# Optimization experiments

Hardware: AMD Instinct MI355X
Metric: run time of the kernel (lower is better)

Reference implementation:

```python
import jax, jax.numpy as jnp
import numpy as np

Cl, Nl, Cv, Nv, M = 32, 128, 8, 64, 500000


def _sample1d(line, g):
    # line: [C, N]; g in [-1,1]; align_corners=True, zeros padding
    C, N = line.shape
    ix = (g + 1.0) * 0.5 * (N - 1)
    i0 = jnp.floor(ix)
    w = ix - i0
    i0 = i0.astype(jnp.int32)
    def gth(i, wt):
        valid = (i >= 0) & (i < N)
        return line[:, jnp.clip(i, 0, N - 1)] * (wt * valid)
    return (gth(i0, 1.0 - w) + gth(i0 + 1, w)).T  # [M, C]


def _sample2d(plane, gx, gy):
    # plane: [C, H, W]; grid x -> W axis, y -> H axis (torch grid_sample convention)
    C, H, W = plane.shape
    ix = (gx + 1.0) * 0.5 * (W - 1)
    iy = (gy + 1.0) * 0.5 * (H - 1)
    x0 = jnp.floor(ix); y0 = jnp.floor(iy)
    wx = ix - x0; wy = iy - y0
    x0 = x0.astype(jnp.int32); y0 = y0.astype(jnp.int32)
    flat = plane.reshape(C, -1)
    def gth(xi, yi, wt):
        valid = (xi >= 0) & (xi < W) & (yi >= 0) & (yi < H)
        idx = jnp.clip(yi, 0, H - 1) * W + jnp.clip(xi, 0, W - 1)
        return flat[:, idx] * (wt * valid)
    out = (gth(x0, y0, (1 - wx) * (1 - wy)) + gth(x0 + 1, y0, wx * (1 - wy))
           + gth(x0, y0 + 1, (1 - wx) * wy) + gth(x0 + 1, y0 + 1, wx * wy))
    return out.T  # [M, C]


def _sample3d(vol, gx, gy, gz):
    # vol: [C, D, H, W]; grid (x,y,z) -> (W,H,D) axes
    C, D, H, W = vol.shape
    ix = (gx + 1.0) * 0.5 * (W - 1)
    iy = (gy + 1.0) * 0.5 * (H - 1)
    iz = (gz + 1.0) * 0.5 * (D - 1)
    x0 = jnp.floor(ix); y0 = jnp.floor(iy); z0 = jnp.floor(iz)
    wx = ix - x0; wy = iy - y0; wz = iz - z0
    x0 = x0.astype(jnp.int32); y0 = y0.astype(jnp.int32); z0 = z0.astype(jnp.int32)
    flat = vol.reshape(C, -1)
    out = 0.0
    for dz in (0, 1):
        for dy in (0, 1):
            for dx in (0, 1):
                xi, yi, zi = x0 + dx, y0 + dy, z0 + dz
                wt = ((wx if dx else 1 - wx) * (wy if dy else 1 - wy) * (wz if dz else 1 - wz))
                valid = (xi >= 0) & (xi < W) & (yi >= 0) & (yi < H) & (zi >= 0) & (zi < D)
                idx = (jnp.clip(zi, 0, D - 1) * H + jnp.clip(yi, 0, H - 1)) * W + jnp.clip(xi, 0, W - 1)
                out = out + flat[:, idx] * (wt * valid)
    return out.T  # [M, C]


def setup_inputs() -> dict:
    key = jax.random.key(0)
    ks = jax.random.split(key, 16)
    rng, shift = 0.4, 0.1
    coordinates = jax.random.uniform(ks[0], (1, M, 3), minval=-1.0, maxval=1.0)
    line_x = jax.random.uniform(ks[1], (Cl, Nl)) * rng + shift
    line_y = jax.random.uniform(ks[2], (Cl, Nl)) * rng + shift
    line_z = jax.random.uniform(ks[3], (Cl, Nl)) * rng + shift
    plane_xy = jax.random.normal(ks[4], (Cl, Nl, Nl)) * rng + shift
    plane_yz = jax.random.normal(ks[5], (Cl, Nl, Nl)) * rng + shift
    plane_xz = jax.random.normal(ks[6], (Cl, Nl, Nl)) * rng + shift
    volume = jax.random.normal(ks[7], (Cv, Nv, Nv, Nv)) * rng + shift
    def lin(k, fi, fo):
        k1, k2 = jax.random.split(k)
        lim = 1.0 / np.sqrt(fi)
        return (jax.random.uniform(k1, (fi, fo), minval=-lim, maxval=lim),
                jax.random.uniform(k2, (fo,), minval=-lim, maxval=lim))
    Wx, bx = lin(ks[8], Cl, Cl)
    Wy, by = lin(ks[9], Cl, Cl)
    Wz, bz = lin(ks[10], Cl, Cl)
    W1, b1 = lin(ks[11], Cl + Cv, 128)
    W2, b2 = lin(ks[12], 128, 1)
    return dict(coordinates=coordinates, line_x=line_x, line_y=line_y, line_z=line_z,
                plane_xy=plane_xy, plane_yz=plane_yz, plane_xz=plane_xz, volume=volume,
                Wx=Wx, bx=bx, Wy=Wy, by=by, Wz=Wz, bz=bz, W1=W1, b1=b1, W2=W2, b2=b2)


def reference(coordinates, line_x, line_y, line_z, plane_xy, plane_yz, plane_xz, volume,
              Wx, bx, Wy, by, Wz, bz, W1, b1, W2, b2):
    c = coordinates[0]  # [M, 3], batch squeezed like the torch code
    x, y, z = c[:, 0], c[:, 1], c[:, 2]
    x_e = _sample1d(line_x, x)
    y_e = _sample1d(line_y, y)
    z_e = _sample1d(line_z, z)
    xy_e = _sample2d(plane_xy, x, y)
    yz_e = _sample2d(plane_yz, y, z)
    xz_e = _sample2d(plane_xz, x, z)
    xyz_e = _sample3d(volume, x, y, z)
    phi = lambda e, W, b: jax.nn.relu(e) @ W + b  # Sequential(ReLU, Linear)
    yztran = phi(yz_e, Wx, bx)
    xztran = phi(xz_e, Wy, by)
    xytran = phi(xy_e, Wz, bz)
    xtran = phi(x_e, Wx, bx)
    ytran = phi(y_e, Wy, by)
    ztran = phi(z_e, Wz, bz)
    features = xtran * yztran + ytran * xztran + ztran * xytran
    features = jnp.concatenate([features, xyz_e], axis=-1)  # [M, Cl+Cv]
    h = jax.nn.relu(features @ W1 + b1)
    return h @ W2 + b2  # [M, 1]
```

## Files before the change

kernel.cpp:

```cpp
#include <hip/hip_runtime.h>

typedef unsigned short u16;
typedef u16 u16x8 __attribute__((ext_vector_type(8)));
typedef _Float16 half2 __attribute__((ext_vector_type(2)));
typedef _Float16 h8v __attribute__((ext_vector_type(8)));
typedef float f4v __attribute__((ext_vector_type(4)));

union H8 { h8v v; half2 p[4]; };

static __device__ __forceinline__ float bf2f(u16 u) {
    union { unsigned int i; float f; } v;
    v.i = ((unsigned int)u) << 16;
    return v.f;
}
static __device__ __forceinline__ u16 f2bf(float f) {
    union { float f; unsigned int i; } v;
    v.f = f;
    unsigned int x = v.i;
    x += 0x7fffu + ((x >> 16) & 1u);
    return (u16)(x >> 16);
}
static __device__ __forceinline__ float gld(int dt, const void* p, int i) {
    return dt ? ((const float*)p)[i] : bf2f(((const u16*)p)[i]);
}
static __device__ __forceinline__ int detect_dt(const void* coords) {
    u16 v = ((const u16*)coords)[threadIdx.x & 63];
    int e = (v >> 7) & 0xFF;
    bool inr = (e >= 90) && (e <= 126);
    unsigned long long m = __ballot(inr);
    return (__popcll(m) >= 56) ? 0 : 1;
}
static __device__ __forceinline__ half2 pk(float a, float b) {
    return __builtin_bit_cast(half2, __builtin_amdgcn_cvt_pkrtz(a, b));
}

static __device__ __forceinline__ void lds_wait() {
    asm volatile("s_waitcnt lgkmcnt(0)" ::: "memory");
}

#define WF_OFF        64u
#define PLANES_S_OFF  34304u
#define VOL_S_OFF     3180032u
#define LINES_S_OFF   7374336u
#define PART_OFF      7398912u
#define TOT_OFF       9496064u
#define ORDER_OFF     9512448u

#define NBUCK 4096
#define HBLOCKS 256

static __device__ __forceinline__ int make_key3(float x, float y, float z) {
    int kx = min(max((int)((x + 1.0f) * 8.0f), 0), 15);
    int ky = min(max((int)((y + 1.0f) * 8.0f), 0), 15);
    int kz = min(max((int)((z + 1.0f) * 8.0f), 0), 15);
    return (kz * 16 + ky) * 16 + kx;
}
static __device__ __forceinline__ int make_key(int dt, const void* coords, int p) {
    return make_key3(gld(dt, coords, p * 3 + 0), gld(dt, coords, p * 3 + 1),
                     gld(dt, coords, p * 3 + 2));
}

static __device__ __forceinline__ void weights_work(
    int dt, int r,
    const void* Wx, const void* bx, const void* Wy, const void* by,
    const void* Wz, const void* bz, const void* W1, const void* b1,
    const void* W2, const void* b2, float* wbase)
{
    _Float16* WtH = (_Float16*)wbase;
    float*    bv  = wbase + 1536;
    _Float16* W1H = (_Float16*)(wbase + 1632);
    float*    b1v = wbase + 5728;
    float*    W2v = wbase + 5856;
    float*    b2v = wbase + 5984;
    if (r < 3072) {
        int m = r >> 10, idx = r & 1023;
        int o = idx >> 5, c = idx & 31;
        const void* s = (m == 0) ? Wx : (m == 1) ? Wy : Wz;
        WtH[r] = (_Float16)gld(dt, s, c * 32 + o);
    } else if (r < 3168) {
        int q2 = r - 3072;
        int m = q2 >> 5, c = q2 & 31;
        const void* s = (m == 0) ? bx : (m == 1) ? by : bz;
        bv[q2] = gld(dt, s, c);
    } else if (r < 11360) {
        int idx = r - 3168;
        int j = idx >> 6, i = idx & 63;
        W1H[idx] = (i < 40) ? (_Float16)gld(dt, W1, i * 128 + j) : (_Float16)0.0f;
    } else if (r < 11488) {
        b1v[r - 11360] = gld(dt, b1, r - 11360);
    } else if (r < 11616) {
        W2v[r - 11488] = gld(dt, W2, r - 11488);
    } else if (r == 11616) {
        b2v[0] = gld(dt, b2, 0);
    }
}

__global__ __launch_bounds__(256) void kp_prep_all(
    const void* __restrict__ coords,
    const void* __restrict__ lx, const void* __restrict__ ly,
    const void* __restrict__ lz,
    const void* __restrict__ pxy, const void* __restrict__ pyz,
    const void* __restrict__ pxz, const void* __restrict__ vol,
    const void* __restrict__ Wx, const void* __restrict__ bx,
    const void* __restrict__ Wy, const void* __restrict__ by,
    const void* __restrict__ Wz, const void* __restrict__ bz,
    const void* __restrict__ W1, const void* __restrict__ b1,
    const void* __restrict__ W2, const void* __restrict__ b2,
    float* __restrict__ wbase,
    u16* __restrict__ planes_s, u16* __restrict__ vol_s,
    u16* __restrict__ lines_s, u16* __restrict__ part, int M)
{
    __shared__ unsigned int lh[NBUCK];
    int dt = detect_dt(coords);
    int blk = blockIdx.x;
    if (blk < 1798) {
        int t = blk * 256 + threadIdx.x;
        u16x8 v;
        if (t < 196608) {
            int o = t * 8;
            int pl = o >> 19;
            int r  = o & 524287;
            int pos = r >> 5, c0 = r & 31;
            const void* src = (pl == 0) ? pxy : (pl == 1) ? pyz : pxz;
#pragma unroll
            for (int i = 0; i < 8; ++i)
                v[i] = dt ? f2bf(((const float*)src)[(c0 + i) * 16384 + pos])
                          : ((const u16*)src)[(c0 + i) * 16384 + pos];
            *(u16x8*)(planes_s + o) = v;
        } else if (t < 458752) {
            int pos = t - 196608;
#pragma unroll
            for (int c = 0; c < 8; ++c)
                v[c] = dt ? f2bf(((const float*)vol)[c * 262144 + pos])
                          : ((const u16*)vol)[c * 262144 + pos];
            *(u16x8*)(vol_s + pos * 8) = v;
        } else {
            int o = (t - 458752) * 8;
            int l = o >> 12, rr = o & 4095;
            int pos = rr >> 5, c0 = rr & 31;
            const void* src = (l == 0) ? lx : (l == 1) ? ly : lz;
#pragma unroll
            for (int i = 0; i < 8; ++i)
                v[i] = dt ? f2bf(((const float*)src)[(c0 + i) * 128 + pos])
                          : ((const u16*)src)[(c0 + i) * 128 + pos];
            *(u16x8*)(lines_s + o) = v;
        }
    } else if (blk < 1844) {
        int r = (blk - 1798) * 256 + threadIdx.x;
        weights_work(dt, r, Wx, bx, Wy, by, Wz, bz, W1, b1, W2, b2, wbase);
    } else {
        int b = blk - 1844;
        for (int i = threadIdx.x; i < NBUCK; i += 256) lh[i] = 0u;
        __syncthreads();
        for (int p = b * 256 + threadIdx.x; p < M; p += HBLOCKS * 256)
            atomicAdd(&lh[make_key(dt, coords, p)], 1u);
        __syncthreads();
        for (int i = threadIdx.x; i < NBUCK; i += 256)
            part[b * NBUCK + i] = (u16)lh[i];
    }
}

__global__ __launch_bounds__(64) void kp_colscan(
    u16* __restrict__ part, unsigned int* __restrict__ tot)
{
    int bkt = blockIdx.x * 64 + threadIdx.x;
    unsigned int run = 0;
#pragma unroll 8
    for (int k = 0; k < HBLOCKS; ++k) {
        unsigned int v = part[k * NBUCK + bkt];
        part[k * NBUCK + bkt] = (u16)run;
        run += v;
    }
    tot[bkt] = run;
}

__global__ __launch_bounds__(256) void kp_scatter_det(
    const void* __restrict__ coords, const u16* __restrict__ part,
    const unsigned int* __restrict__ tot,
    int* __restrict__ order, u16* __restrict__ scoords, int M)
{
    __shared__ unsigned int cnt[NBUCK];
    __shared__ unsigned int psum[256];
    int b = blockIdx.x;
    int t = threadIdx.x;
    unsigned int bs[16];
    unsigned int s = 0;
#pragma unroll
    for (int i = 0; i < 16; ++i) {
        bs[i] = tot[t * 16 + i];
        s += bs[i];
    }
    psum[t] = s;
    __syncthreads();
    if (t == 0) {
        unsigned int run = 0;
        for (int i = 0; i < 256; ++i) { unsigned int v = psum[i]; psum[i] = run; run += v; }
    }
    __syncthreads();
    unsigned int run = psum[t];
#pragma unroll
    for (int i = 0; i < 16; ++i) {
        int bkt = t * 16 + i;
        cnt[bkt] = run + (unsigned int)part[b * NBUCK + bkt];
        run += bs[i];
    }
    __syncthreads();
    int dt = detect_dt(coords);
    const u16* cu = (const u16*)coords;
    for (int p = b * 256 + t; p < M; p += HBLOCKS * 256) {
        float x = gld(dt, coords, p * 3 + 0);
        float y = gld(dt, coords, p * 3 + 1);
        float z = gld(dt, coords, p * 3 + 2);
        int key = make_key3(x, y, z);
        unsigned int pos = atomicAdd(&cnt[key], 1u);
        order[pos] = p;
        if (dt == 0) {
            scoords[pos * 3 + 0] = cu[p * 3 + 0];
            scoords[pos * 3 + 1] = cu[p * 3 + 1];
            scoords[pos * 3 + 2] = cu[p * 3 + 2];
        }
    }
}

struct Samp { int i0, i1; float w0, w1; };

static __device__ __forceinline__ Samp make_samp(float g, int N) {
    float ix = (g + 1.0f) * 0.5f * (float)(N - 1);
    float fl = floorf(ix);
    float w  = ix - fl;
    int i  = (int)fl;
    int i1 = i + 1;
    float v0 = (i  >= 0 && i  < N) ? 1.0f : 0.0f;
    float v1 = (i1 >= 0 && i1 < N) ? 1.0f : 0.0f;
    Samp s;
    s.w0 = (1.0f - w) * v0;
    s.w1 = w * v1;
    s.i0 = min(max(i, 0), N - 1);
    s.i1 = min(max(i1, 0), N - 1);
    return s;
}

#define MFMA16(a, b, c) __builtin_amdgcn_mfma_f32_16x16x32_f16((a), (b), (c), 0, 0, 0)

#define SRE 40
#define SR2 72

struct PL { u16x8 q00[4], q01[4], q10[4], q11[4]; };
struct VL { u16x8 v[8]; };

static __device__ __forceinline__ void plane_load(
    const u16* __restrict__ Ps, const Samp& sa, const Samp& sb, PL& P)
{
    const u16x8* p00 = (const u16x8*)(Ps + (sb.i0 * 128 + sa.i0) * 32);
    const u16x8* p01 = (const u16x8*)(Ps + (sb.i0 * 128 + sa.i1) * 32);
    const u16x8* p10 = (const u16x8*)(Ps + (sb.i1 * 128 + sa.i0) * 32);
    const u16x8* p11 = (const u16x8*)(Ps + (sb.i1 * 128 + sa.i1) * 32);
#pragma unroll
    for (int cc = 0; cc < 4; ++cc) {
        P.q00[cc] = p00[cc]; P.q01[cc] = p01[cc];
        P.q10[cc] = p10[cc]; P.q11[cc] = p11[cc];
    }
}

static __device__ __forceinline__ void vol_loads(
    const u16* __restrict__ vol_s, const Samp& vx, const Samp& vy,
    const Samp& vz, VL& V)
{
#pragma unroll
    for (int corner = 0; corner < 8; ++corner) {
        int dx = corner & 1, dy = (corner >> 1) & 1, dz = corner >> 2;
        int xi = dx ? vx.i1 : vx.i0;
        int yi = dy ? vy.i1 : vy.i0;
        int zi = dz ? vz.i1 : vz.i0;
        V.v[corner] = *(const u16x8*)(vol_s + (((zi * 64) + yi) * 64 + xi) * 8);
    }
}

template<int PRE>
static __device__ __forceinline__ void term_step(
    int lane, int q, int l15,
    const u16* __restrict__ Ls, const Samp& sl,
    const PL& P, const Samp& sa, const Samp& sb,
    const _Float16* __restrict__ Wt, const float* __restrict__ bvt,
    _Float16* El, _Float16* Ep, float (&feat)[4][2][4],
    const u16* __restrict__ nps, const Samp& na, const Samp& nb, PL& PN,
    const u16* __restrict__ vol_s, const Samp& vx, const Samp& vy,
    const Samp& vz, VL& V)
{
    const u16x8* l0 = (const u16x8*)(Ls + sl.i0 * 32);
    const u16x8* l1 = (const u16x8*)(Ls + sl.i1 * 32);
    float w00 = sb.w0 * sa.w0, w01 = sb.w0 * sa.w1;
    float w10 = sb.w1 * sa.w0, w11 = sb.w1 * sa.w1;
#pragma unroll
    for (int cc = 0; cc < 4; ++cc) {
        u16x8 A0 = l0[cc], A1 = l1[cc];
        u16x8 Q00 = P.q00[cc], Q01 = P.q01[cc];
        u16x8 Q10 = P.q10[cc], Q11 = P.q11[cc];
        H8 hl, hp;
#pragma unroll
        for (int kk = 0; kk < 4; ++kk) {
            int k0 = 2 * kk, k1 = k0 + 1;
            float el0 = sl.w0 * bf2f(A0[k0]) + sl.w1 * bf2f(A1[k0]);
            float el1 = sl.w0 * bf2f(A0[k1]) + sl.w1 * bf2f(A1[k1]);
            float ep0 = w00 * bf2f(Q00[k0]) + w01 * bf2f(Q01[k0])
                      + w10 * bf2f(Q10[k0]) + w11 * bf2f(Q11[k0]);
            float ep1 = w00 * bf2f(Q00[k1]) + w01 * bf2f(Q01[k1])
                      + w10 * bf2f(Q10[k1]) + w11 * bf2f(Q11[k1]);
            hl.p[kk] = pk(fmaxf(el0, 0.0f), fmaxf(el1, 0.0f));
            hp.p[kk] = pk(fmaxf(ep0, 0.0f), fmaxf(ep1, 0.0f));
        }
        *(h8v*)&El[lane * SRE + cc * 8] = hl.v;
        *(h8v*)&Ep[lane * SRE + cc * 8] = hp.v;
    }
    if constexpr (PRE == 1) plane_load(nps, na, nb, PN);
    if constexpr (PRE == 2) vol_loads(vol_s, vx, vy, vz, V);

    h8v bf0 = *(const h8v*)&Wt[(l15) * 32 + q * 8];
    h8v bf1 = *(const h8v*)&Wt[(16 + l15) * 32 + q * 8];
    float bb0 = bvt[l15], bb1 = bvt[16 + l15];
    f4v c0 = {bb0, bb0, bb0, bb0};
    f4v c1 = {bb1, bb1, bb1, bb1};
    lds_wait();
#pragma unroll
    for (int mt = 0; mt < 4; ++mt) {
        h8v aL = *(const h8v*)&El[(mt * 16 + l15) * SRE + q * 8];
        h8v aP = *(const h8v*)&Ep[(mt * 16 + l15) * SRE + q * 8];
        f4v ta0 = MFMA16(aL, bf0, c0);
        f4v tb0 = MFMA16(aP, bf0, c0);
        f4v ta1 = MFMA16(aL, bf1, c1);
        f4v tb1 = MFMA16(aP, bf1, c1);
#pragma unroll
        for (int r = 0; r < 4; ++r) {
            feat[mt][0][r] += ta0[r] * tb0[r];
            feat[mt][1][r] += ta1[r] * tb1[r];
        }
    }
    lds_wait();
}

__global__ __launch_bounds__(64) void kp_main_mfma(
    const void* __restrict__ coords, const int* __restrict__ order,
    const u16* __restrict__ scoords,
    const u16* __restrict__ planes_s, const u16* __restrict__ vol_s,
    const u16* __restrict__ lines_s,
    const float* __restrict__ wbase,
    void* __restrict__ out, int M)
{
    __shared__ _Float16 eb[5120];
    __shared__ float res[64];
    int dt = detect_dt(coords);
    const _Float16* WtH = (const _Float16*)wbase;
    const float*    bv  = wbase + 1536;
    const _Float16* W1H = (const _Float16*)(wbase + 1632);
    const float*    b1v = wbase + 5728;
    const float*    W2v = wbase + 5856;
    const float*    b2v = wbase + 5984;

    int lane = threadIdx.x;
    int q = lane >> 4, l15 = lane & 15;
    _Float16* El = eb;
    _Float16* Ep = eb + 2560;
    _Float16* E2 = eb;

    int p = blockIdx.x * 64 + lane;
    p = min(p, M - 1);
    int sp = order[p];

    float x, y, z;
    if (dt == 0) {
        x = bf2f(scoords[p * 3 + 0]);
        y = bf2f(scoords[p * 3 + 1]);
        z = bf2f(scoords[p * 3 + 2]);
    } else {
        x = ((const float*)coords)[sp * 3 + 0];
        y = ((const float*)coords)[sp * 3 + 1];
        z = ((const float*)coords)[sp * 3 + 2];
    }

    Samp sx = make_samp(x, 128), sy = make_samp(y, 128), sz = make_samp(z, 128);

    float feat[4][2][4];
#pragma unroll
    for (int mt = 0; mt < 4; ++mt)
#pragma unroll
        for (int n = 0; n < 2; ++n)
#pragma unroll
            for (int r = 0; r < 4; ++r) feat[mt][n][r] = 0.0f;

    PL Pa, Pb;
    VL V;
    Samp vx, vy, vz;

    plane_load(planes_s + 1 * 524288, sy, sz, Pa);

    term_step<1>(lane, q, l15, lines_s + 0 * 4096, sx, Pa, sy, sz,
                 WtH + 0, bv + 0, El, Ep, feat,
                 planes_s + 2 * 524288, sx, sz, Pb,
                 vol_s, sx, sx, sx, V);

    term_step<1>(lane, q, l15, lines_s + 1 * 4096, sy, Pb, sx, sz,
                 WtH + 1024, bv + 32, El, Ep, feat,
                 planes_s + 0 * 524288, sx, sy, Pa,
                 vol_s, sx, sx, sx, V);

    vx = make_samp(x, 64); vy = make_samp(y, 64); vz = make_samp(z, 64);

    term_step<2>(lane, q, l15, lines_s + 2 * 4096, sz, Pa, sx, sy,
                 WtH + 2048, bv + 64, El, Ep, feat,
                 planes_s, sx, sy, Pb,
                 vol_s, vx, vy, vz, V);

#pragma unroll
    for (int mt = 0; mt < 4; ++mt)
#pragma unroll
        for (int n = 0; n < 2; ++n)
#pragma unroll
            for (int r = 0; r < 4; ++r)
                E2[(mt * 16 + q * 4 + r) * SR2 + n * 16 + l15] =
                    (_Float16)feat[mt][n][r];
    {
        float vf[8];
#pragma unroll
        for (int c = 0; c < 8; ++c) vf[c] = 0.0f;
#pragma unroll
        for (int corner = 0; corner < 8; ++corner) {
            int dx = corner & 1, dy = (corner >> 1) & 1, dz = corner >> 2;
            float w = (dx ? vx.w1 : vx.w0) * (dy ? vy.w1 : vy.w0)
                    * (dz ? vz.w1 : vz.w0);
            u16x8 v = V.v[corner];
#pragma unroll
            for (int c = 0; c < 8; ++c)
                vf[c] = fmaf(w, bf2f(v[c]), vf[c]);
        }
        H8 hv;
#pragma unroll
        for (int k = 0; k < 4; ++k) hv.p[k] = pk(vf[2 * k], vf[2 * k + 1]);
        *(h8v*)&E2[lane * SR2 + 32] = hv.v;
        h8v zz = {};
        *(h8v*)&E2[lane * SR2 + 40] = zz;
        *(h8v*)&E2[lane * SR2 + 48] = zz;
        *(h8v*)&E2[lane * SR2 + 56] = zz;
    }
    lds_wait();

    h8v af[4][2];
#pragma unroll
    for (int mt = 0; mt < 4; ++mt)
#pragma unroll
        for (int ks = 0; ks < 2; ++ks)
            af[mt][ks] = *(const h8v*)&E2[(mt * 16 + l15) * SR2 + ks * 32 + q * 8];

    float s[4][4];
#pragma unroll
    for (int mt = 0; mt < 4; ++mt)
#pragma unroll
        for (int r = 0; r < 4; ++r) s[mt][r] = 0.0f;

#pragma unroll
    for (int NT = 0; NT < 8; ++NT) {
        int o = NT * 16 + l15;
        h8v b0  = *(const h8v*)&W1H[o * 64 + q * 8];
        h8v b1f = *(const h8v*)&W1H[o * 64 + 32 + q * 8];
        float w2 = W2v[o];
        float bb = b1v[o];
        f4v cinit = {bb, bb, bb, bb};
#pragma unroll
        for (int mt = 0; mt < 4; ++mt) {
            f4v c = MFMA16(af[mt][0], b0, cinit);
            c = MFMA16(af[mt][1], b1f, c);
#pragma unroll
            for (int r = 0; r < 4; ++r)
                s[mt][r] = fmaf(fmaxf(c[r], 0.0f), w2, s[mt][r]);
        }
    }
#pragma unroll
    for (int mt = 0; mt < 4; ++mt)
#pragma unroll
        for (int r = 0; r < 4; ++r) {
            float v = s[mt][r];
            v += __shfl_xor(v, 1);
            v += __shfl_xor(v, 2);
            v += __shfl_xor(v, 4);
            v += __shfl_xor(v, 8);
            s[mt][r] = v;
        }
    if (l15 == 0) {
#pragma unroll
        for (int mt = 0; mt < 4; ++mt)
#pragma unroll
            for (int r = 0; r < 4; ++r)
                res[mt * 16 + q * 4 + r] = s[mt][r];
    }
    lds_wait();
    float rr = res[lane] + b2v[0];
    if (dt) ((float*)out)[sp] = rr;
    else    ((u16*)out)[sp] = f2bf(rr);
}

__global__ void kp_prep_weights_fb(
    const void* __restrict__ coords,
    const void* __restrict__ Wx, const void* __restrict__ bx,
    const void* __restrict__ Wy, const void* __restrict__ by,
    const void* __restrict__ Wz, const void* __restrict__ bz,
    const void* __restrict__ W1, const void* __restrict__ b1,
    const void* __restrict__ W2, const void* __restrict__ b2,
    float* __restrict__ wbase)
{
    int dt = detect_dt(coords);
    int t = blockIdx.x * blockDim.x + threadIdx.x;
    weights_work(dt, t, Wx, bx, Wy, by, Wz, bz, W1, b1, W2, b2, wbase);
}

__global__ __launch_bounds__(256) void kp_main_direct(
    const void* __restrict__ coords,
    const void* __restrict__ lx, const void* __restrict__ ly, const void* __restrict__ lz,
    const void* __restrict__ pxy, const void* __restrict__ pyz, const void* __restrict__ pxz,
    const void* __restrict__ vol,
    const float* __restrict__ wbase,
    void* __restrict__ out, int M)
{
    int dt = detect_dt(coords);
    const _Float16* WtH = (const _Float16*)wbase;
    const float*    bv  = wbase + 1536;
    const _Float16* W1H = (const _Float16*)(wbase + 1632);
    const float*    b1v = wbase + 5728;
    const float*    W2v = wbase + 5856;
    const float*    b2v = wbase + 5984;

    int p = blockIdx.x * 256 + threadIdx.x;
    p = min(p, M - 1);

    float x = gld(dt, coords, p * 3 + 0);
    float y = gld(dt, coords, p * 3 + 1);
    float z = gld(dt, coords, p * 3 + 2);

    Samp sx = make_samp(x, 128), sy = make_samp(y, 128), sz = make_samp(z, 128);

    float feat[40];
#pragma unroll
    for (int o = 0; o < 40; ++o) feat[o] = 0.0f;

    const void* Ls[3] = {lx, ly, lz};
    const void* Psv[3] = {pyz, pxz, pxy};
    Samp sl3[3] = {sx, sy, sz};
    Samp sa3[3] = {sy, sx, sx};
    Samp sb3[3] = {sz, sz, sy};
#pragma unroll 1
    for (int m = 0; m < 3; ++m) {
        float ta[32], tb[32];
        const float* bvt = bv + m * 32;
        const _Float16* Wt = WtH + m * 1024;
#pragma unroll
        for (int o = 0; o < 32; ++o) { ta[o] = bvt[o]; tb[o] = bvt[o]; }
        Samp sl = sl3[m], sa = sa3[m], sb = sb3[m];
        float w00 = sb.w0 * sa.w0, w01 = sb.w0 * sa.w1;
        float w10 = sb.w1 * sa.w0, w11 = sb.w1 * sa.w1;
        int i00 = sb.i0 * 128 + sa.i0, i01 = sb.i0 * 128 + sa.i1;
        int i10 = sb.i1 * 128 + sa.i0, i11 = sb.i1 * 128 + sa.i1;
#pragma unroll 1
        for (int c = 0; c < 32; ++c) {
            float el = sl.w0 * gld(dt, Ls[m], c * 128 + sl.i0)
                     + sl.w1 * gld(dt, Ls[m], c * 128 + sl.i1);
            float ep = w00 * gld(dt, Psv[m], c * 16384 + i00)
                     + w01 * gld(dt, Psv[m], c * 16384 + i01)
                     + w10 * gld(dt, Psv[m], c * 16384 + i10)
                     + w11 * gld(dt, Psv[m], c * 16384 + i11);
            float r1 = fmaxf(el, 0.0f), r2 = fmaxf(ep, 0.0f);
#pragma unroll
            for (int o = 0; o < 32; ++o) {
                float w = (float)Wt[o * 32 + c];
                ta[o] = fmaf(r1, w, ta[o]);
                tb[o] = fmaf(r2, w, tb[o]);
            }
        }
#pragma unroll
        for (int o = 0; o < 32; ++o) feat[o] = fmaf(ta[o], tb[o], feat[o]);
    }

    Samp vx = make_samp(x, 64), vy = make_samp(y, 64), vz = make_samp(z, 64);
#pragma unroll 1
    for (int corner = 0; corner < 8; ++corner) {
        int dx = corner & 1, dy = (corner >> 1) & 1, dz = corner >> 2;
        int xi = dx ? vx.i1 : vx.i0;
        int yi = dy ? vy.i1 : vy.i0;
        int zi = dz ? vz.i1 : vz.i0;
        float w = (dx ? vx.w1 : vx.w0) * (dy ? vy.w1 : vy.w0) * (dz ? vz.w1 : vz.w0);
        int pos = ((zi * 64) + yi) * 64 + xi;
#pragma unroll
        for (int c = 0; c < 8; ++c)
            feat[32 + c] = fmaf(w, gld(dt, vol, c * 262144 + pos), feat[32 + c]);
    }

    float acc_out = b2v[0];
#pragma unroll 2
    for (int j = 0; j < 128; ++j) {
        float acc = b1v[j];
        const _Float16* wr = W1H + j * 64;
#pragma unroll
        for (int i = 0; i < 40; ++i)
            acc = fmaf(feat[i], (float)wr[i], acc);
        acc_out = fmaf(fmaxf(acc, 0.0f), W2v[j], acc_out);
    }
    if (dt) ((float*)out)[p] = acc_out;
    else    ((u16*)out)[p] = f2bf(acc_out);
}

extern "C" void kernel_launch(void* const* d_in, const int* in_sizes, int n_in,
                              void* d_out, int out_size, void* d_ws, size_t ws_size,
                              hipStream_t stream) {
    const void* coords = d_in[0];
    const void* lx  = d_in[1];
    const void* ly  = d_in[2];
    const void* lz  = d_in[3];
    const void* pxy = d_in[4];
    const void* pyz = d_in[5];
    const void* pxz = d_in[6];
    const void* vol = d_in[7];
    const void* Wx  = d_in[8];
    const void* bx  = d_in[9];
    const void* Wy  = d_in[10];
    const void* by  = d_in[11];
    const void* Wz  = d_in[12];
    const void* bz  = d_in[13];
    const void* W1  = d_in[14];
    const void* b1  = d_in[15];
    const void* W2  = d_in[16];
    const void* b2  = d_in[17];

    int M = in_sizes[0] / 3;

    char* ws = (char*)d_ws;
    float*        wbase    = (float*)(ws + WF_OFF);
    u16*          planes_s = (u16*)(ws + PLANES_S_OFF);
    u16*          vol_s    = (u16*)(ws + VOL_S_OFF);
    u16*          lines_s  = (u16*)(ws + LINES_S_OFF);
    u16*          part     = (u16*)(ws + PART_OFF);
    unsigned int* tot      = (unsigned int*)(ws + TOT_OFF);
    int*          order    = (int*)(ws + ORDER_OFF);
    u16*          scoords  = (u16*)(ws + ORDER_OFF + (size_t)M * 4u);

    size_t need_sorted = (size_t)ORDER_OFF + (size_t)M * 4u + (size_t)M * 6u;

    if (ws_size >= need_sorted) {
        kp_prep_all<<<2100, 256, 0, stream>>>(coords, lx, ly, lz, pxy, pyz, pxz, vol,
                                              Wx, bx, Wy, by, Wz, bz, W1, b1, W2, b2,
                                              wbase, planes_s, vol_s, lines_s, part, M);
        kp_colscan<<<64, 64, 0, stream>>>(part, tot);
        kp_scatter_det<<<HBLOCKS, 256, 0, stream>>>(coords, part, tot, order,
                                                    scoords, M);
        int blocks64 = (M + 63) / 64;
        kp_main_mfma<<<blocks64, 64, 0, stream>>>(coords, order, scoords,
                                                  planes_s, vol_s,
                                                  lines_s, wbase, d_out, M);
    } else {
        int blocks = (M + 255) / 256;
        kp_prep_weights_fb<<<46, 256, 0, stream>>>(coords, Wx, bx, Wy, by, Wz, bz,
                                                   W1, b1, W2, b2, wbase);
        kp_main_direct<<<blocks, 256, 0, stream>>>(coords, lx, ly, lz, pxy, pyz, pxz,
                                                   vol, wbase, d_out, M);
    }
}
```

Before: 199.4 us.

## Parallelize histogram column scan and block prefix with wave-level scans

The column scan kernel, which walked all HBLOCKS partial counts serially per bucket with only 64 threads per block, is replaced by one wavefront per bucket that loads four counts per lane and runs a shuffle-based inclusive scan. The single-thread serial 256-entry prefix in the scatter kernel becomes a log-step LDS scan with barriers. LDS row strides for the embedding staging buffers shrink, reducing shared memory per block in the main kernel. The new column scan assumes HBLOCKS equals 256, and the stride change could alter LDS bank-conflict behaviour.

```diff
diff --git a/kernel.cpp b/kernel.cpp
--- a/kernel.cpp
+++ b/kernel.cpp
@@ -160,18 +160,31 @@
     }
 }
 
-__global__ __launch_bounds__(64) void kp_colscan(
+__global__ __launch_bounds__(256) void kp_colscan(
     u16* __restrict__ part, unsigned int* __restrict__ tot)
 {
-    int bkt = blockIdx.x * 64 + threadIdx.x;
-    unsigned int run = 0;
-#pragma unroll 8
-    for (int k = 0; k < HBLOCKS; ++k) {
-        unsigned int v = part[k * NBUCK + bkt];
-        part[k * NBUCK + bkt] = (u16)run;
-        run += v;
-    }
-    tot[bkt] = run;
+    int lane = threadIdx.x & 63;
+    int bkt  = blockIdx.x * 4 + (threadIdx.x >> 6);
+    unsigned int v[4];
+    unsigned int ltot = 0;
+#pragma unroll
+    for (int i = 0; i < 4; ++i) {
+        v[i] = part[(lane * 4 + i) * NBUCK + bkt];
+        ltot += v[i];
+    }
+    unsigned int x = ltot;
+#pragma unroll
+    for (int d = 1; d < 64; d <<= 1) {
+        unsigned int y = __shfl_up(x, d);
+        if (lane >= d) x += y;
+    }
+    unsigned int run = x - ltot;
+#pragma unroll
+    for (int i = 0; i < 4; ++i) {
+        part[(lane * 4 + i) * NBUCK + bkt] = (u16)run;
+        run += v[i];
+    }
+    if (lane == 63) tot[bkt] = x;
 }
 
 __global__ __launch_bounds__(256) void kp_scatter_det(
@@ -192,12 +205,14 @@
     }
     psum[t] = s;
     __syncthreads();
-    if (t == 0) {
-        unsigned int run = 0;
-        for (int i = 0; i < 256; ++i) { unsigned int v = psum[i]; psum[i] = run; run += v; }
-    }
-    __syncthreads();
-    unsigned int run = psum[t];
+#pragma unroll
+    for (int d = 1; d < 256; d <<= 1) {
+        unsigned int v = (t >= d) ? psum[t - d] : 0u;
+        __syncthreads();
+        psum[t] += v;
+        __syncthreads();
+    }
+    unsigned int run = psum[t] - s;
 #pragma unroll
     for (int i = 0; i < 16; ++i) {
         int bkt = t * 16 + i;
@@ -242,8 +257,8 @@
 
 #define MFMA16(a, b, c) __builtin_amdgcn_mfma_f32_16x16x32_f16((a), (b), (c), 0, 0, 0)
 
-#define SRE 40
-#define SR2 72
+#define SRE 34
+#define SR2 68
 
 struct PL { u16x8 q00[4], q01[4], q10[4], q11[4]; };
 struct VL { u16x8 v[8]; };
@@ -346,7 +361,7 @@
     const float* __restrict__ wbase,
     void* __restrict__ out, int M)
 {
-    __shared__ _Float16 eb[5120];
+    __shared__ _Float16 eb[2 * 64 * SRE];
     __shared__ float res[64];
     int dt = detect_dt(coords);
     const _Float16* WtH = (const _Float16*)wbase;
@@ -359,7 +374,7 @@
     int lane = threadIdx.x;
     int q = lane >> 4, l15 = lane & 15;
     _Float16* El = eb;
-    _Float16* Ep = eb + 2560;
+    _Float16* Ep = eb + 64 * SRE;
     _Float16* E2 = eb;
 
     int p = blockIdx.x * 64 + lane;
@@ -645,7 +660,7 @@
         kp_prep_all<<<2100, 256, 0, stream>>>(coords, lx, ly, lz, pxy, pyz, pxz, vol,
                                               Wx, bx, Wy, by, Wz, bz, W1, b1, W2, b2,
                                               wbase, planes_s, vol_s, lines_s, part, M);
-        kp_colscan<<<64, 64, 0, stream>>>(part, tot);
+        kp_colscan<<<NBUCK / 4, 256, 0, stream>>>(part, tot);
         kp_scatter_det<<<HBLOCKS, 256, 0, stream>>>(coords, part, tot, order,
                                                     scoords, M);
         int blocks64 = (M + 63) / 64;
```

New measurement: 206.8 us. 1.04x slower.

## Remove spatial bucket sort and process points in original order

Applied to the files above, without the earlier changes.

Drops the histogram, column-scan and scatter kernels that reordered points into spatial buckets, and has the main MFMA kernel read coordinates and write outputs directly by point index. This removes two launches plus the sorting traffic over all points. The cost is that gathers from the planes and volume lose spatial coherence within a wavefront, which may raise cache misses in the sampling stage.

```diff
diff --git a/kernel.cpp b/kernel.cpp
--- a/kernel.cpp
+++ b/kernel.cpp
@@ -42,23 +42,7 @@
 #define PLANES_S_OFF  34304u
 #define VOL_S_OFF     3180032u
 #define LINES_S_OFF   7374336u
-#define PART_OFF      7398912u
-#define TOT_OFF       9496064u
-#define ORDER_OFF     9512448u
-
-#define NBUCK 4096
-#define HBLOCKS 256
-
-static __device__ __forceinline__ int make_key3(float x, float y, float z) {
-    int kx = min(max((int)((x + 1.0f) * 8.0f), 0), 15);
-    int ky = min(max((int)((y + 1.0f) * 8.0f), 0), 15);
-    int kz = min(max((int)((z + 1.0f) * 8.0f), 0), 15);
-    return (kz * 16 + ky) * 16 + kx;
-}
-static __device__ __forceinline__ int make_key(int dt, const void* coords, int p) {
-    return make_key3(gld(dt, coords, p * 3 + 0), gld(dt, coords, p * 3 + 1),
-                     gld(dt, coords, p * 3 + 2));
-}
+#define WS_NEED       7398912u
 
 static __device__ __forceinline__ void weights_work(
     int dt, int r,
@@ -108,9 +92,8 @@
     const void* __restrict__ W2, const void* __restrict__ b2,
     float* __restrict__ wbase,
     u16* __restrict__ planes_s, u16* __restrict__ vol_s,
-    u16* __restrict__ lines_s, u16* __restrict__ part, int M)
-{
-    __shared__ unsigned int lh[NBUCK];
+    u16* __restrict__ lines_s)
+{
     int dt = detect_dt(coords);
     int blk = blockIdx.x;
     if (blk < 1798) {
@@ -145,80 +128,9 @@
                           : ((const u16*)src)[(c0 + i) * 128 + pos];
             *(u16x8*)(lines_s + o) = v;
         }
-    } else if (blk < 1844) {
+    } else {
         int r = (blk - 1798) * 256 + threadIdx.x;
         weights_work(dt, r, Wx, bx, Wy, by, Wz, bz, W1, b1, W2, b2, wbase);
-    } else {
-        int b = blk - 1844;
-        for (int i = threadIdx.x; i < NBUCK; i += 256) lh[i] = 0u;
-        __syncthreads();
-        for (int p = b * 256 + threadIdx.x; p < M; p += HBLOCKS * 256)
-            atomicAdd(&lh[make_key(dt, coords, p)], 1u);
-        __syncthreads();
-        for (int i = threadIdx.x; i < NBUCK; i += 256)
-            part[b * NBUCK + i] = (u16)lh[i];
-    }
-}
-
-__global__ __launch_bounds__(64) void kp_colscan(
-    u16* __restrict__ part, unsigned int* __restrict__ tot)
-{
-    int bkt = blockIdx.x * 64 + threadIdx.x;
-    unsigned int run = 0;
-#pragma unroll 8
-    for (int k = 0; k < HBLOCKS; ++k) {
-        unsigned int v = part[k * NBUCK + bkt];
-        part[k * NBUCK + bkt] = (u16)run;
-        run += v;
-    }
-    tot[bkt] = run;
-}
-
-__global__ __launch_bounds__(256) void kp_scatter_det(
-    const void* __restrict__ coords, const u16* __restrict__ part,
-    const unsigned int* __restrict__ tot,
-    int* __restrict__ order, u16* __restrict__ scoords, int M)
-{
-    __shared__ unsigned int cnt[NBUCK];
-    __shared__ unsigned int psum[256];
-    int b = blockIdx.x;
-    int t = threadIdx.x;
-    unsigned int bs[16];
-    unsigned int s = 0;
-#pragma unroll
-    for (int i = 0; i < 16; ++i) {
-        bs[i] = tot[t * 16 + i];
-        s += bs[i];
-    }
-    psum[t] = s;
-    __syncthreads();
-    if (t == 0) {
-        unsigned int run = 0;
-        for (int i = 0; i < 256; ++i) { unsigned int v = psum[i]; psum[i] = run; run += v; }
-    }
-    __syncthreads();
-    unsigned int run = psum[t];
-#pragma unroll
-    for (int i = 0; i < 16; ++i) {
-        int bkt = t * 16 + i;
-        cnt[bkt] = run + (unsigned int)part[b * NBUCK + bkt];
-        run += bs[i];
-    }
-    __syncthreads();
-    int dt = detect_dt(coords);
-    const u16* cu = (const u16*)coords;
-    for (int p = b * 256 + t; p < M; p += HBLOCKS * 256) {
-        float x = gld(dt, coords, p * 3 + 0);
-        float y = gld(dt, coords, p * 3 + 1);
-        float z = gld(dt, coords, p * 3 + 2);
-        int key = make_key3(x, y, z);
-        unsigned int pos = atomicAdd(&cnt[key], 1u);
-        order[pos] = p;
-        if (dt == 0) {
-            scoords[pos * 3 + 0] = cu[p * 3 + 0];
-            scoords[pos * 3 + 1] = cu[p * 3 + 1];
-            scoords[pos * 3 + 2] = cu[p * 3 + 2];
-        }
     }
 }
 
@@ -339,8 +251,7 @@
 }
 
 __global__ __launch_bounds__(64) void kp_main_mfma(
-    const void* __restrict__ coords, const int* __restrict__ order,
-    const u16* __restrict__ scoords,
+    const void* __restrict__ coords,
     const u16* __restrict__ planes_s, const u16* __restrict__ vol_s,
     const u16* __restrict__ lines_s,
     const float* __restrict__ wbase,
@@ -364,17 +275,17 @@
 
     int p = blockIdx.x * 64 + lane;
     p = min(p, M - 1);
-    int sp = order[p];
 
     float x, y, z;
     if (dt == 0) {
-        x = bf2f(scoords[p * 3 + 0]);
-        y = bf2f(scoords[p * 3 + 1]);
-        z = bf2f(scoords[p * 3 + 2]);
+        const u16* cu = (const u16*)coords;
+        x = bf2f(cu[p * 3 + 0]);
+        y = bf2f(cu[p * 3 + 1]);
+        z = bf2f(cu[p * 3 + 2]);
     } else {
-        x = ((const float*)coords)[sp * 3 + 0];
-        y = ((const float*)coords)[sp * 3 + 1];
-        z = ((const float*)coords)[sp * 3 + 2];
+        x = ((const float*)coords)[p * 3 + 0];
+        y = ((const float*)coords)[p * 3 + 1];
+        z = ((const float*)coords)[p * 3 + 2];
     }
 
     Samp sx = make_samp(x, 128), sy = make_samp(y, 128), sz = make_samp(z, 128);
@@ -493,8 +404,8 @@
     }
     lds_wait();
     float rr = res[lane] + b2v[0];
-    if (dt) ((float*)out)[sp] = rr;
-    else    ((u16*)out)[sp] = f2bf(rr);
+    if (dt) ((float*)out)[p] = rr;
+    else    ((u16*)out)[p]   = f2bf(rr);
 }
 
 __global__ void kp_prep_weights_fb(
@@ -630,28 +541,18 @@
     int M = in_sizes[0] / 3;
 
     char* ws = (char*)d_ws;
-    float*        wbase    = (float*)(ws + WF_OFF);
-    u16*          planes_s = (u16*)(ws + PLANES_S_OFF);
-    u16*          vol_s    = (u16*)(ws + VOL_S_OFF);
-    u16*          lines_s  = (u16*)(ws + LINES_S_OFF);
-    u16*          part     = (u16*)(ws + PART_OFF);
-    unsigned int* tot      = (unsigned int*)(ws + TOT_OFF);
-    int*          order    = (int*)(ws + ORDER_OFF);
-    u16*          scoords  = (u16*)(ws + ORDER_OFF + (size_t)M * 4u);
-
-    size_t need_sorted = (size_t)ORDER_OFF + (size_t)M * 4u + (size_t)M * 6u;
-
-    if (ws_size >= need_sorted) {
-        kp_prep_all<<<2100, 256, 0, stream>>>(coords, lx, ly, lz, pxy, pyz, pxz, vol,
+    float* wbase    = (float*)(ws + WF_OFF);
+    u16*   planes_s = (u16*)(ws + PLANES_S_OFF);
+    u16*   vol_s    = (u16*)(ws + VOL_S_OFF);
+    u16*   lines_s  = (u16*)(ws + LINES_S_OFF);
+
+    if (ws_size >= (size_t)WS_NEED) {
+        kp_prep_all<<<1844, 256, 0, stream>>>(coords, lx, ly, lz, pxy, pyz, pxz, vol,
                                               Wx, bx, Wy, by, Wz, bz, W1, b1, W2, b2,
-                                              wbase, planes_s, vol_s, lines_s, part, M);
-        kp_colscan<<<64, 64, 0, stream>>>(part, tot);
-        kp_scatter_det<<<HBLOCKS, 256, 0, stream>>>(coords, part, tot, order,
-                                                    scoords, M);
+                                              wbase, planes_s, vol_s, lines_s);
         int blocks64 = (M + 63) / 64;
-        kp_main_mfma<<<blocks64, 64, 0, stream>>>(coords, order, scoords,
-                                                  planes_s, vol_s,
-                                                  lines_s, wbase, d_out, M);
+        kp_main_mfma<<<blocks64, 64, 0, stream>>>(coords, planes_s, vol_s, lines_s,
+                                                  wbase, d_out, M);
     } else {
         int blocks = (M + 255) / 256;
         kp_prep_weights_fb<<<46, 256, 0, stream>>>(coords, Wx, bx, Wy, by, Wz, bz,
```

New measurement: 194.3 us (median of 2 runs). -2.6%, faster.
